# Kernel optimization log

Hardware: AMD Instinct MI355X
Metric: run time of the kernel (lower is better)

The kernel has to match this reference:

```python
import jax, jax.numpy as jnp
import numpy as np

B, S, D, H = 4, 2048, 1024, 16
DH = D // H
NEG = -100000.0


def setup_inputs() -> dict:
    key = jax.random.key(0)
    ks = jax.random.split(key, 13)
    s = 1.0 / np.sqrt(D)
    inp = {
        'q': jax.random.normal(ks[0], (B, S, D), jnp.float32),
        'k': jax.random.normal(ks[1], (B, S, D), jnp.float32),
        'v': jax.random.normal(ks[2], (B, S, D), jnp.float32),
        'mask': jax.random.randint(ks[3], (B, 1, S, S), 0, 2).astype(bool),
        'wq_w': jax.random.normal(ks[4], (D, D), jnp.float32) * s,
        'wq_b': jnp.zeros((D,), jnp.float32),
        'wk_w': jax.random.normal(ks[5], (D, D), jnp.float32) * s,
        'wk_b': jnp.zeros((D,), jnp.float32),
        'wv_w': jax.random.normal(ks[6], (D, D), jnp.float32) * s,
        'wv_b': jnp.zeros((D,), jnp.float32),
        'wo_w': jax.random.normal(ks[7], (D, D), jnp.float32) * s,
        'wo_b': jnp.zeros((D,), jnp.float32),
    }
    return inp


def reference(q, k, v, mask, wq_w, wq_b, wk_w, wk_b, wv_w, wv_b, wo_w, wo_b):
    # torch Linear: y = x @ W^T + b
    qh = (q @ wq_w.T + wq_b).reshape(B, S, H, DH).transpose(0, 2, 1, 3)  # [B,H,S,DH]
    kh = (k @ wk_w.T + wk_b).reshape(B, S, H, DH).transpose(0, 2, 1, 3)
    vh = (v @ wv_w.T + wv_b).reshape(B, S, H, DH).transpose(0, 2, 1, 3)
    # NOTE: original code has NO 1/sqrt(d) scaling
    alpha = jnp.einsum('bhqd,bhkd->bhqk', qh, kh)  # [B,H,S,S]
    alpha = jnp.where(mask, NEG, alpha)
    score = jax.nn.softmax(alpha, axis=-1)
    x = jnp.einsum('bhqk,bhkd->bhqd', score, vh)
    x = x.transpose(0, 2, 1, 3).reshape(B, S, D)
    return x @ wo_w.T + wo_b
```

## Files before the change

kernel.cpp:

```cpp
#include <hip/hip_runtime.h>
#include <hip/hip_bf16.h>

#define B_ 4
#define S_ 2048
#define D_ 1024
#define H_ 16
#define NEGV (-100000.0f)
#define L2E 1.4426950408889634f

typedef __attribute__((ext_vector_type(8))) short short8;
typedef __attribute__((ext_vector_type(4))) float f32x4;
typedef unsigned short us;
typedef unsigned long long u64;

__device__ __forceinline__ us f2h(float f) {
  union { _Float16 h; us u; } c;
  c.h = (_Float16)f;
  return c.u;
}
__device__ __forceinline__ float exp2a(float x) {
  float r;
  asm("v_exp_f32 %0, %1" : "=v"(r) : "v"(x));
  return r;
}

__global__ void detect_mask_kernel(const int* __restrict__ mi, int* __restrict__ flag) {
  int t = threadIdx.x;
  bool bad = false;
  for (int i = t; i < 16384; i += 64) {
    int v = mi[i];
    bad = bad || (v != 0 && v != 1);
  }
  unsigned long long any = __ballot(bad);
  if (t == 0) flag[0] = (any != 0ull) ? 1 : 0;
}

__global__ __launch_bounds__(256) void pack_mask(const void* __restrict__ maskp,
                                                 const int* __restrict__ flag,
                                                 unsigned* __restrict__ pk) {
  int w = blockIdx.x * 256 + threadIdx.x;
  unsigned bits = 0;
  if (flag[0]) {
    const uint4* p = (const uint4*)((const unsigned char*)maskp + (size_t)w * 32);
#pragma unroll
    for (int q = 0; q < 2; ++q) {
      uint4 v = p[q];
      unsigned vv[4] = {v.x, v.y, v.z, v.w};
#pragma unroll
      for (int e = 0; e < 4; ++e) {
        unsigned byte4 = vv[e];
#pragma unroll
        for (int bb = 0; bb < 4; ++bb)
          bits |= (unsigned)(((byte4 >> (8 * bb)) & 0xffu) != 0) << (q * 16 + e * 4 + bb);
      }
    }
  } else {
    const uint4* p = (const uint4*)((const int*)maskp + (size_t)w * 32);
#pragma unroll
    for (int q = 0; q < 8; ++q) {
      uint4 v = p[q];
      bits |= (unsigned)(v.x != 0) << (q * 4 + 0);
      bits |= (unsigned)(v.y != 0) << (q * 4 + 1);
      bits |= (unsigned)(v.z != 0) << (q * 4 + 2);
      bits |= (unsigned)(v.w != 0) << (q * 4 + 3);
    }
  }
  pk[w] = bits;
}

__global__ __launch_bounds__(256) void cvt_f16x3(const float* __restrict__ i0,
                                                 const float* __restrict__ i1,
                                                 const float* __restrict__ i2,
                                                 us* __restrict__ o0, us* __restrict__ o1,
                                                 us* __restrict__ o2) {
  int z = blockIdx.x >> 12;
  int i = (blockIdx.x & 4095) * 256 + threadIdx.x;
  const float* in = z == 0 ? i0 : z == 1 ? i1 : i2;
  us* out = z == 0 ? o0 : z == 1 ? o1 : o2;
  float4 a = ((const float4*)in)[2 * i];
  float4 b = ((const float4*)in)[2 * i + 1];
  us u[8] = {f2h(a.x), f2h(a.y), f2h(a.z), f2h(a.w),
             f2h(b.x), f2h(b.y), f2h(b.z), f2h(b.w)};
  ((uint4*)out)[i] = *(uint4*)u;
}

__global__ __launch_bounds__(256) void cvt_w4(const float* __restrict__ w0,
                                              const float* __restrict__ w1,
                                              const float* __restrict__ w2,
                                              const float* __restrict__ w3,
                                              us* __restrict__ d0, us* __restrict__ d1,
                                              us* __restrict__ d2, us* __restrict__ d3) {
  int which = blockIdx.x >> 9;
  int i = (blockIdx.x & 511) * 256 + threadIdx.x;
  const float* w = which == 0 ? w0 : which == 1 ? w1 : which == 2 ? w2 : w3;
  us* d = which == 0 ? d0 : which == 1 ? d1 : which == 2 ? d2 : d3;
  float4 a = ((const float4*)w)[2 * i];
  float4 b = ((const float4*)w)[2 * i + 1];
  us u[8] = {f2h(a.x), f2h(a.y), f2h(a.z), f2h(a.w),
             f2h(b.x), f2h(b.y), f2h(b.z), f2h(b.w)};
  ((uint4*)d)[i] = *(uint4*)u;
}

__device__ __forceinline__ void gload16(const us* g, us* l) {
  __builtin_amdgcn_global_load_lds((const __attribute__((address_space(1))) void*)g,
                                   (__attribute__((address_space(3))) void*)l, 16, 0, 0);
}

__device__ __forceinline__ int swzb(int row, int c16) {
  return row * 128 + ((c16 ^ (row & 7)) << 4);
}

template <int OMODE>
__global__ __launch_bounds__(256) void gemm_mfma(
    const us* __restrict__ A0, const us* __restrict__ A1, const us* __restrict__ A2,
    const us* __restrict__ Wp0, const us* __restrict__ Wp1, const us* __restrict__ Wp2,
    const float* __restrict__ b0, const float* __restrict__ b1, const float* __restrict__ b2,
    void* __restrict__ C0, void* __restrict__ C1, void* __restrict__ C2,
    int M, int N, int K) {
  __shared__ __align__(16) us As[2][128 * 64];
  __shared__ __align__(16) us Ws[2][128 * 64];

  const int z = blockIdx.z;
  const us* A = z == 0 ? A0 : z == 1 ? A1 : A2;
  const us* W = z == 0 ? Wp0 : z == 1 ? Wp1 : Wp2;
  const float* bias = z == 0 ? b0 : z == 1 ? b1 : b2;
  void* Cp = z == 0 ? C0 : z == 1 ? C1 : C2;

  const int m0 = blockIdx.x * 128;
  const int n0 = blockIdx.y * 128;
  const int t = threadIdx.x;
  const int w = t >> 6, l = t & 63;
  const int l15 = l & 15, l4 = l >> 4;
  const int wm = w >> 1, wn = w & 1;

  int goff[4];
#pragma unroll
  for (int j = 0; j < 4; ++j) {
    int u = t + j * 256;
    int r = u >> 3, c8 = u & 7;
    int g = c8 ^ (r & 7);
    goff[j] = r * K + g * 8;
  }
  const us* Ag = A + (size_t)m0 * K;
  const us* Wg = W + (size_t)n0 * K;

  f32x4 acc[4][4];
#pragma unroll
  for (int m = 0; m < 4; ++m)
#pragma unroll
    for (int n = 0; n < 4; ++n) acc[m][n] = (f32x4){0.f, 0.f, 0.f, 0.f};

  auto stage = [&](int k0, int bb) {
#pragma unroll
    for (int j = 0; j < 4; ++j) {
      int u = t + j * 256;
      gload16(Ag + goff[j] + k0, &As[bb][u * 8]);
      gload16(Wg + goff[j] + k0, &Ws[bb][u * 8]);
    }
  };

  stage(0, 0);
  __syncthreads();
  int cur = 0;
  for (int k0 = 0; k0 < K; k0 += 64) {
    if (k0 + 64 < K) stage(k0 + 64, cur ^ 1);
#pragma unroll
    for (int ks = 0; ks < 2; ++ks) {
      short8 ah[4], bh_[4];
#pragma unroll
      for (int m = 0; m < 4; ++m)
        ah[m] = *(const short8*)((const char*)As[cur] + swzb(wm * 64 + m * 16 + l15, ks * 4 + l4));
#pragma unroll
      for (int n = 0; n < 4; ++n)
        bh_[n] = *(const short8*)((const char*)Ws[cur] + swzb(wn * 64 + n * 16 + l15, ks * 4 + l4));
#pragma unroll
      for (int m = 0; m < 4; ++m)
#pragma unroll
        for (int n = 0; n < 4; ++n)
          acc[m][n] = __builtin_amdgcn_mfma_f32_16x16x32_f16(ah[m], bh_[n], acc[m][n], 0, 0, 0);
    }
    __syncthreads();
    cur ^= 1;
  }

  float bv[4];
#pragma unroll
  for (int n = 0; n < 4; ++n) bv[n] = bias[n0 + wn * 64 + n * 16 + l15];

#pragma unroll
  for (int m = 0; m < 4; ++m) {
#pragma unroll
    for (int i = 0; i < 4; ++i) {
      int gm = m0 + wm * 64 + m * 16 + l4 * 4 + i;
#pragma unroll
      for (int n = 0; n < 4; ++n) {
        int gn = n0 + wn * 64 + n * 16 + l15;
        float o = acc[m][n][i] + bv[n];
        if constexpr (OMODE == 0) {
          ((float*)Cp)[(size_t)gm * N + gn] = o;
        } else {
          int b = gm >> 11, s = gm & (S_ - 1);
          int hh = gn >> 6, d = gn & 63;
          size_t idx = (((size_t)(b * H_ + hh) << 11) + s) * 64 + d;
          ((us*)Cp)[idx] = f2h(o);
        }
      }
    }
  }
}

__global__ __launch_bounds__(256) void transpose_v(const us* __restrict__ vh,
                                                   us* __restrict__ vt) {
  __shared__ us Ts[64][72];
  int blk = blockIdx.x;
  int bh = blk >> 5, s0 = (blk & 31) << 6;
  int t = threadIdx.x;
#pragma unroll
  for (int p = 0; p < 2; ++p) {
    int c = t + p * 256;
    int rs = c >> 3, c8 = c & 7;
    *(uint4*)&Ts[rs][c8 * 8] = *(const uint4*)(vh + ((size_t)bh * S_ + s0 + rs) * 64 + c8 * 8);
  }
  __syncthreads();
#pragma unroll
  for (int p = 0; p < 2; ++p) {
    int c = t + p * 256;
    int rd = c >> 3, s8 = c & 7;
    union { us u[8]; uint4 v; } tmp;
#pragma unroll
    for (int e = 0; e < 8; ++e) tmp.u[e] = Ts[s8 * 8 + e][rd];
    *(uint4*)(vt + ((size_t)bh * 64 + rd) * S_ + s0 + s8 * 8) = tmp.v;
  }
}

__device__ __forceinline__ int swz(int row, int bc) {
  return (row << 7) + (bc ^ ((row & 7) << 4));
}

__global__ __launch_bounds__(512) void attn_mfma(
    const us* __restrict__ qh, const us* __restrict__ kh,
    const us* __restrict__ vt, const unsigned* __restrict__ pk,
    us* __restrict__ xout) {
  __shared__ __align__(16) us Ks[2][4096];
  __shared__ __align__(16) us Vs[2][4096];
  __shared__ __align__(16) char Ps[16384];

  const int blk = ((blockIdx.x & 7) << 7) + (blockIdx.x >> 3);
  const int bh = blk >> 4;
  const int q0 = (blk & 15) << 7;
  const int b = bh >> 4, h = bh & (H_ - 1);
  const int t = threadIdx.x;
  const int w = t >> 6, l = t & 63;
  const int l15 = l & 15, l4 = l >> 4;

  short8 qf[2];
  {
    const size_t qbase = ((size_t)bh * S_ + q0 + 16 * w + l15) * 64 + l4 * 8;
    qf[0] = *(const short8*)(qh + qbase);
    qf[1] = *(const short8*)(qh + qbase + 32);
  }

  f32x4 accO[4];
#pragma unroll
  for (int jd = 0; jd < 4; ++jd) accO[jd] = (f32x4){0.f, 0.f, 0.f, 0.f};
  float m_i = -1e30f, l_p = 0.f;

  const int r_st = t >> 3, c_st = (t & 7) ^ ((t >> 3) & 7);
  const us* kh_src = kh + ((size_t)bh * S_ + r_st) * 64 + c_st * 8;
  const us* vt_src = vt + ((size_t)bh * 64 + r_st) * S_ + c_st * 8;

  auto stage = [&](int k0, int bb) {
    gload16(kh_src + (size_t)k0 * 64, &Ks[bb][t * 8]);
    gload16(vt_src + k0, &Vs[bb][t * 8]);
  };

  stage(0, 0);
  __syncthreads();
  int cur = 0;

  char* Pw = Ps + w * 2048;
  const int prowb = l15 * 128;
  const int rr7 = l15 & 7;
  const int bhalf = l4 >> 1;
  const int wsub = (l4 & 1) * 8;
  const unsigned* pb = pk + ((size_t)b * S_ + q0 + 16 * w + l15) * (S_ / 32);

  for (int k0 = 0; k0 < S_; k0 += 64) {
    uint2 mw = *(const uint2*)(pb + (k0 >> 5));
    if (k0 + 64 < S_) stage(k0 + 64, cur ^ 1);

    const char* KT = (const char*)Ks[cur];
    const char* VT = (const char*)Vs[cur];

    __builtin_amdgcn_s_setprio(1);
    f32x4 sj[4];
#pragma unroll
    for (int j = 0; j < 4; ++j) {
      f32x4 s = {0.f, 0.f, 0.f, 0.f};
#pragma unroll
      for (int c = 0; c < 2; ++c) {
        short8 kf = *(const short8*)(KT + swz(l15 + 16 * j, l4 * 16 + 64 * c));
        s = __builtin_amdgcn_mfma_f32_16x16x32_f16(kf, qf[c], s, 0, 0, 0);
      }
      sj[j] = s;
    }
    __builtin_amdgcn_s_setprio(0);

    float tm = -3e38f;
#pragma unroll
    for (int j = 0; j < 4; ++j) {
      unsigned wrd = (j < 2) ? mw.x : mw.y;
      int bb = ((j & 1) << 4) + (l4 << 2);
#pragma unroll
      for (int i = 0; i < 4; ++i) {
        float bf = (float)((wrd >> (bb + i)) & 1u);
        sj[j][i] = fmaf(bf, NEGV, sj[j][i]);
      }
      tm = fmaxf(tm, fmaxf(fmaxf(sj[j][0], sj[j][1]), fmaxf(sj[j][2], sj[j][3])));
    }
    tm = fmaxf(tm, __shfl_xor(tm, 16));
    tm = fmaxf(tm, __shfl_xor(tm, 32));

    if (__any(tm - m_i > 8.0f)) {
      float mnew = fmaxf(m_i, tm);
      float scl = exp2a((m_i - mnew) * L2E);
      l_p *= scl;
      m_i = mnew;
      float sr0 = __shfl(scl, 4 * l4 + 0);
      float sr1 = __shfl(scl, 4 * l4 + 1);
      float sr2 = __shfl(scl, 4 * l4 + 2);
      float sr3 = __shfl(scl, 4 * l4 + 3);
#pragma unroll
      for (int jd = 0; jd < 4; ++jd) {
        accO[jd][0] *= sr0; accO[jd][1] *= sr1;
        accO[jd][2] *= sr2; accO[jd][3] *= sr3;
      }
    }

    float ml2 = m_i * L2E;
#pragma unroll
    for (int j = 0; j < 4; ++j) {
      float p0 = exp2a(fmaf(sj[j][0], L2E, -ml2));
      float p1 = exp2a(fmaf(sj[j][1], L2E, -ml2));
      float p2 = exp2a(fmaf(sj[j][2], L2E, -ml2));
      float p3 = exp2a(fmaf(sj[j][3], L2E, -ml2));
      l_p += (p0 + p1) + (p2 + p3);
      unsigned d0, d1;
      asm("v_cvt_pkrtz_f16_f32 %0, %1, %2" : "=v"(d0) : "v"(p0), "v"(p1));
      asm("v_cvt_pkrtz_f16_f32 %0, %1, %2" : "=v"(d1) : "v"(p2), "v"(p3));
      int chunk = ((j << 1) | bhalf) ^ rr7;
      *(u64*)(Pw + prowb + (chunk << 4) + wsub) = (u64)d0 | ((u64)d1 << 32);
    }
    asm volatile("s_waitcnt lgkmcnt(0)" ::: "memory");
    __builtin_amdgcn_sched_barrier(0);

    __builtin_amdgcn_s_setprio(1);
#pragma unroll
    for (int kc = 0; kc < 2; ++kc) {
      int chR = (4 * kc + l4) ^ rr7;
      short8 pa = *(const short8*)(Pw + prowb + (chR << 4));
#pragma unroll
      for (int jd = 0; jd < 4; ++jd) {
        short8 vb = *(const short8*)(VT + swz(l15 + 16 * jd, l4 * 16 + 64 * kc));
        accO[jd] = __builtin_amdgcn_mfma_f32_16x16x32_f16(pa, vb, accO[jd], 0, 0, 0);
      }
    }
    __builtin_amdgcn_s_setprio(0);
    __syncthreads();
    cur ^= 1;
  }

  float lr = l_p;
  lr += __shfl_xor(lr, 16);
  lr += __shfl_xor(lr, 32);
  float inv0 = 1.f / __shfl(lr, 4 * l4 + 0);
  float inv1 = 1.f / __shfl(lr, 4 * l4 + 1);
  float inv2 = 1.f / __shfl(lr, 4 * l4 + 2);
  float inv3 = 1.f / __shfl(lr, 4 * l4 + 3);
  float invs[4] = {inv0, inv1, inv2, inv3};
#pragma unroll
  for (int i = 0; i < 4; ++i) {
    int row = q0 + 16 * w + l4 * 4 + i;
    size_t obase = ((size_t)b * S_ + row) * D_ + h * 64 + l15;
#pragma unroll
    for (int jd = 0; jd < 4; ++jd) xout[obase + 16 * jd] = f2h(accO[jd][i] * invs[i]);
  }
}

extern "C" void kernel_launch(void* const* d_in, const int* in_sizes, int n_in,
                              void* d_out, int out_size, void* d_ws, size_t ws_size,
                              hipStream_t stream) {
  const float* q = (const float*)d_in[0];
  const float* k = (const float*)d_in[1];
  const float* v = (const float*)d_in[2];
  const void* mask = d_in[3];
  const float* wq_w = (const float*)d_in[4];
  const float* wq_b = (const float*)d_in[5];
  const float* wk_w = (const float*)d_in[6];
  const float* wk_b = (const float*)d_in[7];
  const float* wv_w = (const float*)d_in[8];
  const float* wv_b = (const float*)d_in[9];
  const float* wo_w = (const float*)d_in[10];
  const float* wo_b = (const float*)d_in[11];

  const size_t NE = (size_t)B_ * S_ * D_;
  const size_t NW = (size_t)D_ * D_;
  const size_t PKB = (size_t)(B_ * S_ * (S_ / 32)) * 4;
  char* ws = (char*)d_ws;
  int* flag = (int*)ws;
  unsigned* pkb = (unsigned*)(ws + 256);
  us* base = (us*)(ws + 256 + PKB);

  detect_mask_kernel<<<1, 64, 0, stream>>>((const int*)mask, flag);
  pack_mask<<<2048, 256, 0, stream>>>(mask, flag, pkb);

  dim3 g2(64, 8, 2);
  dim3 g3(64, 8, 3);
  dim3 g1(64, 8, 1);

  const size_t fused_need = 256 + PKB + 6 * NE * 2 + 4 * NW * 2;
  if (ws_size >= fused_need) {
    us* A0 = base;
    us* A1 = A0 + NE;
    us* A2 = A1 + NE;
    us* A3 = A2 + NE;
    us* A4 = A3 + NE;
    us* A5 = A4 + NE;
    us* W0 = A5 + NE;
    us* W1 = W0 + NW;
    us* W2 = W1 + NW;
    us* W3 = W2 + NW;
    cvt_w4<<<2048, 256, 0, stream>>>(wq_w, wk_w, wv_w, wo_w, W0, W1, W2, W3);
    cvt_f16x3<<<3 * 4096, 256, 0, stream>>>(q, k, v, A0, A1, A2);
    gemm_mfma<2><<<g3, 256, 0, stream>>>(A0, A1, A2, W0, W1, W2, wq_b, wk_b, wv_b,
                                         A3, A4, A5, B_ * S_, D_, D_);
    transpose_v<<<2048, 256, 0, stream>>>(A5, A0);
    attn_mfma<<<1024, 512, 0, stream>>>(A3, A4, A0, pkb, A1);
    gemm_mfma<0><<<g1, 256, 0, stream>>>(A1, A1, A1, W3, W3, W3, wo_b, wo_b, wo_b,
                                         d_out, d_out, d_out, B_ * S_, D_, D_);
  } else {
    us* A0 = base;
    us* A1 = A0 + NE;
    us* A2 = A1 + NE;
    us* A3 = A2 + NE;
    us* A4 = A3 + NE;
    us* W0 = A4 + NE;
    us* W1 = W0 + NW;
    us* W2 = W1 + NW;
    us* W3 = W2 + NW;
    cvt_w4<<<2048, 256, 0, stream>>>(wq_w, wk_w, wv_w, wo_w, W0, W1, W2, W3);
    cvt_f16x3<<<2 * 4096, 256, 0, stream>>>(q, k, nullptr, A0, A1, nullptr);
    gemm_mfma<2><<<g2, 256, 0, stream>>>(A0, A1, nullptr, W0, W1, nullptr, wq_b, wk_b, nullptr,
                                         A2, A3, nullptr, B_ * S_, D_, D_);
    cvt_f16x3<<<4096, 256, 0, stream>>>(v, nullptr, nullptr, A0, nullptr, nullptr);
    gemm_mfma<2><<<g1, 256, 0, stream>>>(A0, nullptr, nullptr, W2, nullptr, nullptr,
                                         wv_b, nullptr, nullptr, A1, nullptr, nullptr,
                                         B_ * S_, D_, D_);
    transpose_v<<<2048, 256, 0, stream>>>(A1, A4);
    attn_mfma<<<1024, 512, 0, stream>>>(A2, A3, A4, pkb, A0);
    gemm_mfma<0><<<g1, 256, 0, stream>>>(A0, nullptr, nullptr, W3, nullptr, nullptr,
                                         wo_b, nullptr, nullptr, d_out, nullptr, nullptr,
                                         B_ * S_, D_, D_);
  }
}
```

Measured before the change: 364.1 us.

## Use 256x256 GEMM tiles with 4-stage pipeline and streamline attention masking

Replaces the 128x128 double-buffered projection GEMM with a 256x256-tile, 512-thread kernel. It uses a 4-deep ring of K=32 stages synchronized by explicit vmcnt waits and raw barriers, to raise data reuse and hide global-load latency. In attention, mask application uses a shared 16-entry nibble lookup table of float4 offsets instead of per-element bit extraction, and the row max is computed as a flatter tree. The softmax row-sum is now accumulated in packed fp16, which cuts VALU work but lowers the precision of the denominator. The GEMM grid drops to 128 blocks per projection, which may underfill the GPU's compute units.

```diff
diff --git a/kernel.cpp b/kernel.cpp
--- a/kernel.cpp
+++ b/kernel.cpp
@@ -10,6 +10,7 @@
 
 typedef __attribute__((ext_vector_type(8))) short short8;
 typedef __attribute__((ext_vector_type(4))) float f32x4;
+typedef _Float16 hf2 __attribute__((ext_vector_type(2)));
 typedef unsigned short us;
 typedef unsigned long long u64;
 
@@ -106,19 +107,14 @@
                                    (__attribute__((address_space(3))) void*)l, 16, 0, 0);
 }
 
-__device__ __forceinline__ int swzb(int row, int c16) {
-  return row * 128 + ((c16 ^ (row & 7)) << 4);
-}
-
 template <int OMODE>
-__global__ __launch_bounds__(256) void gemm_mfma(
+__global__ __launch_bounds__(512, 1) void gemm256(
     const us* __restrict__ A0, const us* __restrict__ A1, const us* __restrict__ A2,
     const us* __restrict__ Wp0, const us* __restrict__ Wp1, const us* __restrict__ Wp2,
     const float* __restrict__ b0, const float* __restrict__ b1, const float* __restrict__ b2,
     void* __restrict__ C0, void* __restrict__ C1, void* __restrict__ C2,
     int M, int N, int K) {
-  __shared__ __align__(16) us As[2][128 * 64];
-  __shared__ __align__(16) us Ws[2][128 * 64];
+  __shared__ __align__(16) us SM[4][16384];
 
   const int z = blockIdx.z;
   const us* A = z == 0 ? A0 : z == 1 ? A1 : A2;
@@ -126,72 +122,94 @@
   const float* bias = z == 0 ? b0 : z == 1 ? b1 : b2;
   void* Cp = z == 0 ? C0 : z == 1 ? C1 : C2;
 
-  const int m0 = blockIdx.x * 128;
-  const int n0 = blockIdx.y * 128;
+  const int m0 = blockIdx.x * 256;
+  const int n0 = blockIdx.y * 256;
   const int t = threadIdx.x;
   const int w = t >> 6, l = t & 63;
   const int l15 = l & 15, l4 = l >> 4;
-  const int wm = w >> 1, wn = w & 1;
-
-  int goff[4];
-#pragma unroll
-  for (int j = 0; j < 4; ++j) {
-    int u = t + j * 256;
-    int r = u >> 3, c8 = u & 7;
-    int g = c8 ^ (r & 7);
+  const int wm = w >> 2, wn = w & 3;
+
+  int goff[2];
+#pragma unroll
+  for (int j = 0; j < 2; ++j) {
+    int u = t + j * 512;
+    int r = u >> 2, c4 = u & 3;
+    int g = c4 ^ (r & 3);
     goff[j] = r * K + g * 8;
   }
   const us* Ag = A + (size_t)m0 * K;
   const us* Wg = W + (size_t)n0 * K;
 
-  f32x4 acc[4][4];
-#pragma unroll
-  for (int m = 0; m < 4; ++m)
+  f32x4 acc[8][4];
+#pragma unroll
+  for (int m = 0; m < 8; ++m)
 #pragma unroll
     for (int n = 0; n < 4; ++n) acc[m][n] = (f32x4){0.f, 0.f, 0.f, 0.f};
 
-  auto stage = [&](int k0, int bb) {
-#pragma unroll
-    for (int j = 0; j < 4; ++j) {
-      int u = t + j * 256;
-      gload16(Ag + goff[j] + k0, &As[bb][u * 8]);
-      gload16(Wg + goff[j] + k0, &Ws[bb][u * 8]);
+  auto stage = [&](int kt, int bb) {
+#pragma unroll
+    for (int j = 0; j < 2; ++j) {
+      int u = t + j * 512;
+      gload16(Ag + goff[j] + kt * 32, &SM[bb][u * 8]);
+    }
+#pragma unroll
+    for (int j = 0; j < 2; ++j) {
+      int u = t + j * 512;
+      gload16(Wg + goff[j] + kt * 32, &SM[bb][8192 + u * 8]);
     }
   };
 
+  auto body = [&](int bb) {
+    const char* Ab = (const char*)&SM[bb][0];
+    const char* Bb = Ab + 16384;
+    short8 bf[4];
+#pragma unroll
+    for (int n = 0; n < 4; ++n) {
+      int row = wn * 64 + n * 16 + l15;
+      bf[n] = *(const short8*)(Bb + row * 64 + ((l4 ^ (row & 3)) << 4));
+    }
+#pragma unroll
+    for (int m = 0; m < 8; ++m) {
+      int row = wm * 128 + m * 16 + l15;
+      short8 af = *(const short8*)(Ab + row * 64 + ((l4 ^ (row & 3)) << 4));
+#pragma unroll
+      for (int n = 0; n < 4; ++n)
+        acc[m][n] = __builtin_amdgcn_mfma_f32_16x16x32_f16(af, bf[n], acc[m][n], 0, 0, 0);
+    }
+  };
+
+  const int nt = K / 32;
   stage(0, 0);
-  __syncthreads();
-  int cur = 0;
-  for (int k0 = 0; k0 < K; k0 += 64) {
-    if (k0 + 64 < K) stage(k0 + 64, cur ^ 1);
-#pragma unroll
-    for (int ks = 0; ks < 2; ++ks) {
-      short8 ah[4], bh_[4];
-#pragma unroll
-      for (int m = 0; m < 4; ++m)
-        ah[m] = *(const short8*)((const char*)As[cur] + swzb(wm * 64 + m * 16 + l15, ks * 4 + l4));
-#pragma unroll
-      for (int n = 0; n < 4; ++n)
-        bh_[n] = *(const short8*)((const char*)Ws[cur] + swzb(wn * 64 + n * 16 + l15, ks * 4 + l4));
-#pragma unroll
-      for (int m = 0; m < 4; ++m)
-#pragma unroll
-        for (int n = 0; n < 4; ++n)
-          acc[m][n] = __builtin_amdgcn_mfma_f32_16x16x32_f16(ah[m], bh_[n], acc[m][n], 0, 0, 0);
-    }
-    __syncthreads();
-    cur ^= 1;
-  }
+  stage(1, 1);
+  stage(2, 2);
+  int tt = 0;
+  for (; tt < nt - 3; ++tt) {
+    asm volatile("s_waitcnt vmcnt(8)" ::: "memory");
+    asm volatile("s_barrier" ::: "memory");
+    stage(tt + 3, (tt + 3) & 3);
+    body(tt & 3);
+  }
+  asm volatile("s_waitcnt vmcnt(8)" ::: "memory");
+  asm volatile("s_barrier" ::: "memory");
+  body(tt & 3);
+  ++tt;
+  asm volatile("s_waitcnt vmcnt(4)" ::: "memory");
+  asm volatile("s_barrier" ::: "memory");
+  body(tt & 3);
+  ++tt;
+  asm volatile("s_waitcnt vmcnt(0)" ::: "memory");
+  asm volatile("s_barrier" ::: "memory");
+  body(tt & 3);
 
   float bv[4];
 #pragma unroll
   for (int n = 0; n < 4; ++n) bv[n] = bias[n0 + wn * 64 + n * 16 + l15];
 
 #pragma unroll
-  for (int m = 0; m < 4; ++m) {
+  for (int m = 0; m < 8; ++m) {
 #pragma unroll
     for (int i = 0; i < 4; ++i) {
-      int gm = m0 + wm * 64 + m * 16 + l4 * 4 + i;
+      int gm = m0 + wm * 128 + m * 16 + l4 * 4 + i;
 #pragma unroll
       for (int n = 0; n < 4; ++n) {
         int gn = n0 + wn * 64 + n * 16 + l15;
@@ -244,6 +262,7 @@
   __shared__ __align__(16) us Ks[2][4096];
   __shared__ __align__(16) us Vs[2][4096];
   __shared__ __align__(16) char Ps[16384];
+  __shared__ __align__(16) float MLutF[64];
 
   const int blk = ((blockIdx.x & 7) << 7) + (blockIdx.x >> 3);
   const int bh = blk >> 4;
@@ -274,6 +293,7 @@
     gload16(vt_src + k0, &Vs[bb][t * 8]);
   };
 
+  if (t < 64) MLutF[t] = (((t >> 2) >> (t & 3)) & 1) ? NEGV : 0.f;
   stage(0, 0);
   __syncthreads();
   int cur = 0;
@@ -306,18 +326,20 @@
     }
     __builtin_amdgcn_s_setprio(0);
 
-    float tm = -3e38f;
 #pragma unroll
     for (int j = 0; j < 4; ++j) {
       unsigned wrd = (j < 2) ? mw.x : mw.y;
-      int bb = ((j & 1) << 4) + (l4 << 2);
-#pragma unroll
-      for (int i = 0; i < 4; ++i) {
-        float bf = (float)((wrd >> (bb + i)) & 1u);
-        sj[j][i] = fmaf(bf, NEGV, sj[j][i]);
-      }
-      tm = fmaxf(tm, fmaxf(fmaxf(sj[j][0], sj[j][1]), fmaxf(sj[j][2], sj[j][3])));
-    }
+      unsigned nib = (wrd >> (((j & 1) << 4) + (l4 << 2))) & 0xFu;
+      f32x4 lv = *(const f32x4*)&MLutF[nib << 2];
+      sj[j] = sj[j] + lv;
+    }
+
+    float c0 = fmaxf(fmaxf(sj[0][0], sj[0][1]), sj[0][2]);
+    float c1 = fmaxf(fmaxf(sj[0][3], sj[1][0]), sj[1][1]);
+    float c2 = fmaxf(fmaxf(sj[1][2], sj[1][3]), sj[2][0]);
+    float c3 = fmaxf(fmaxf(sj[2][1], sj[2][2]), sj[2][3]);
+    float c4 = fmaxf(fmaxf(sj[3][0], sj[3][1]), sj[3][2]);
+    float tm = fmaxf(fmaxf(fmaxf(c0, c1), c2), fmaxf(fmaxf(c3, c4), sj[3][3]));
     tm = fmaxf(tm, __shfl_xor(tm, 16));
     tm = fmaxf(tm, __shfl_xor(tm, 32));
 
@@ -338,19 +360,26 @@
     }
 
     float ml2 = m_i * L2E;
+    hf2 acc2;
+    acc2.x = (_Float16)0.f;
+    acc2.y = (_Float16)0.f;
 #pragma unroll
     for (int j = 0; j < 4; ++j) {
       float p0 = exp2a(fmaf(sj[j][0], L2E, -ml2));
       float p1 = exp2a(fmaf(sj[j][1], L2E, -ml2));
       float p2 = exp2a(fmaf(sj[j][2], L2E, -ml2));
       float p3 = exp2a(fmaf(sj[j][3], L2E, -ml2));
-      l_p += (p0 + p1) + (p2 + p3);
       unsigned d0, d1;
       asm("v_cvt_pkrtz_f16_f32 %0, %1, %2" : "=v"(d0) : "v"(p0), "v"(p1));
       asm("v_cvt_pkrtz_f16_f32 %0, %1, %2" : "=v"(d1) : "v"(p2), "v"(p3));
+      union { unsigned u; hf2 h; } c0u, c1u;
+      c0u.u = d0;
+      c1u.u = d1;
+      acc2 = acc2 + c0u.h + c1u.h;
       int chunk = ((j << 1) | bhalf) ^ rr7;
       *(u64*)(Pw + prowb + (chunk << 4) + wsub) = (u64)d0 | ((u64)d1 << 32);
     }
+    l_p += (float)acc2.x + (float)acc2.y;
     asm volatile("s_waitcnt lgkmcnt(0)" ::: "memory");
     __builtin_amdgcn_sched_barrier(0);
 
@@ -414,9 +443,9 @@
   detect_mask_kernel<<<1, 64, 0, stream>>>((const int*)mask, flag);
   pack_mask<<<2048, 256, 0, stream>>>(mask, flag, pkb);
 
-  dim3 g2(64, 8, 2);
-  dim3 g3(64, 8, 3);
-  dim3 g1(64, 8, 1);
+  dim3 g3(32, 4, 3);
+  dim3 g2(32, 4, 2);
+  dim3 g1(32, 4, 1);
 
   const size_t fused_need = 256 + PKB + 6 * NE * 2 + 4 * NW * 2;
   if (ws_size >= fused_need) {
@@ -432,12 +461,12 @@
     us* W3 = W2 + NW;
     cvt_w4<<<2048, 256, 0, stream>>>(wq_w, wk_w, wv_w, wo_w, W0, W1, W2, W3);
     cvt_f16x3<<<3 * 4096, 256, 0, stream>>>(q, k, v, A0, A1, A2);
-    gemm_mfma<2><<<g3, 256, 0, stream>>>(A0, A1, A2, W0, W1, W2, wq_b, wk_b, wv_b,
-                                         A3, A4, A5, B_ * S_, D_, D_);
+    gemm256<2><<<g3, 512, 0, stream>>>(A0, A1, A2, W0, W1, W2, wq_b, wk_b, wv_b,
+                                       A3, A4, A5, B_ * S_, D_, D_);
     transpose_v<<<2048, 256, 0, stream>>>(A5, A0);
     attn_mfma<<<1024, 512, 0, stream>>>(A3, A4, A0, pkb, A1);
-    gemm_mfma<0><<<g1, 256, 0, stream>>>(A1, A1, A1, W3, W3, W3, wo_b, wo_b, wo_b,
-                                         d_out, d_out, d_out, B_ * S_, D_, D_);
+    gemm256<0><<<g1, 512, 0, stream>>>(A1, A1, A1, W3, W3, W3, wo_b, wo_b, wo_b,
+                                       d_out, d_out, d_out, B_ * S_, D_, D_);
   } else {
     us* A0 = base;
     us* A1 = A0 + NE;
@@ -450,16 +479,16 @@
     us* W3 = W2 + NW;
     cvt_w4<<<2048, 256, 0, stream>>>(wq_w, wk_w, wv_w, wo_w, W0, W1, W2, W3);
     cvt_f16x3<<<2 * 4096, 256, 0, stream>>>(q, k, nullptr, A0, A1, nullptr);
-    gemm_mfma<2><<<g2, 256, 0, stream>>>(A0, A1, nullptr, W0, W1, nullptr, wq_b, wk_b, nullptr,
-                                         A2, A3, nullptr, B_ * S_, D_, D_);
+    gemm256<2><<<g2, 512, 0, stream>>>(A0, A1, nullptr, W0, W1, nullptr, wq_b, wk_b, nullptr,
+                                       A2, A3, nullptr, B_ * S_, D_, D_);
     cvt_f16x3<<<4096, 256, 0, stream>>>(v, nullptr, nullptr, A0, nullptr, nullptr);
-    gemm_mfma<2><<<g1, 256, 0, stream>>>(A0, nullptr, nullptr, W2, nullptr, nullptr,
-                                         wv_b, nullptr, nullptr, A1, nullptr, nullptr,
-                                         B_ * S_, D_, D_);
+    gemm256<2><<<g1, 512, 0, stream>>>(A0, nullptr, nullptr, W2, nullptr, nullptr,
+                                       wv_b, nullptr, nullptr, A1, nullptr, nullptr,
+                                       B_ * S_, D_, D_);
     transpose_v<<<2048, 256, 0, stream>>>(A1, A4);
     attn_mfma<<<1024, 512, 0, stream>>>(A2, A3, A4, pkb, A0);
-    gemm_mfma<0><<<g1, 256, 0, stream>>>(A0, nullptr, nullptr, W3, nullptr, nullptr,
-                                         wo_b, nullptr, nullptr, d_out, nullptr, nullptr,
-                                         B_ * S_, D_, D_);
-  }
-}
+    gemm256<0><<<g1, 512, 0, stream>>>(A0, nullptr, nullptr, W3, nullptr, nullptr,
+                                       wo_b, nullptr, nullptr, d_out, nullptr, nullptr,
+                                       B_ * S_, D_, D_);
+  }
+}
```

Result: no change. 364.4 us (+0.1%).
